# Kernel optimization log

Measured on AMD Instinct MI355X. Metric: run time of the kernel, lower is better.

## Reference

```python
import jax, jax.numpy as jnp
import numpy as np
from jax.scipy.linalg import expm

DELTA = 0.01  # time step from __init__ delta
B_SZ, U_DIM, DU_DIM, H_DIM, Y_DIM = 512, 1024, 512, 2048, 1024


def setup_inputs() -> dict:
    key = jax.random.key(0)
    ks = jax.random.split(key, 6)
    inv_sqrt = lambda fan_in: 1.0 / np.sqrt(fan_in)
    u = jax.random.normal(ks[0], (B_SZ, U_DIM), jnp.float32)
    du = jax.random.normal(ks[1], (B_SZ, DU_DIM), jnp.float32)
    # torch.nn.Linear default init: U(-1/sqrt(fan_in), 1/sqrt(fan_in))
    W = jax.random.uniform(ks[2], (H_DIM, H_DIM), jnp.float32, -inv_sqrt(H_DIM), inv_sqrt(H_DIM))
    Bw = jax.random.uniform(ks[3], (H_DIM, U_DIM + DU_DIM), jnp.float32, -inv_sqrt(U_DIM + DU_DIM), inv_sqrt(U_DIM + DU_DIM))
    Cw = jax.random.uniform(ks[4], (Y_DIM, H_DIM), jnp.float32, -inv_sqrt(H_DIM), inv_sqrt(H_DIM))
    h = jax.random.normal(ks[5], (1, H_DIM), jnp.float32)
    return {"u": u, "du": du, "W": W, "Bw": Bw, "Cw": Cw, "h": h}


def reference(u, du, W, Bw, Cw, h):
    # Antisymmetric part of W
    A = 0.5 * (W - W.T)                                    # (H,H)
    A_expm = expm(A * DELTA)                               # (H,H) matrix exponential
    rec = h @ A_expm.T                                     # (1,H) recurrent term: F.linear(h, A_expm)
    A_inv = jnp.linalg.inv(A)                              # (H,H)
    # B(cat([du, u])) : (B, H)
    b = jnp.concatenate([du, u], axis=1) @ Bw.T
    # M = A^{-1} (expm(A*delta) - I); input term = M @ b^T per sample -> b @ M^T
    M = A_inv @ (A_expm - jnp.eye(H_DIM, dtype=A.dtype))   # (H,H)
    inp = b @ M.T                                          # (B,H)
    h_new = rec + inp                                      # broadcast (1,H)+(B,H) -> (B,H)
    y = h_new @ Cw.T                                       # (B,Y)
    return y
```

## Files before the change

kernel.cpp:

```cpp
#include <hip/hip_runtime.h>
#include <hip/hip_bf16.h>


#define B_SZ 512
#define U_DIM 1024
#define DU_DIM 512
#define H_DIM 2048
#define Y_DIM 1024
#define K_CAT 1536
#define DELTA_F 0.01f

typedef __hip_bfloat16 bf16;
using bf16x8f = __attribute__((ext_vector_type(8))) short;
using f32x4   = __attribute__((ext_vector_type(4))) float;

__device__ __forceinline__ short f2bs(float x) {
  union { bf16 b; short s; } u; u.b = __float2bfloat16(x); return u.s;
}
__device__ __forceinline__ int4 pack8(const float4 v0, const float4 v1) {
  union { short s[8]; int4 i; } o;
  o.s[0] = f2bs(v0.x); o.s[1] = f2bs(v0.y); o.s[2] = f2bs(v0.z); o.s[3] = f2bs(v0.w);
  o.s[4] = f2bs(v1.x); o.s[5] = f2bs(v1.y); o.s[6] = f2bs(v1.z); o.s[7] = f2bs(v1.w);
  return o.i;
}

#define LDP 72
#define LDS_SHORTS (2 * 32 * LDP + 2 * 64 * LDP)

#define NB (H_DIM * K_CAT / 8)

__global__ __launch_bounds__(256) void k1(const float* __restrict__ W, const float* __restrict__ h,
                                          const float* __restrict__ Bw, float* __restrict__ wh,
                                          float* __restrict__ wtp, short* __restrict__ Bwb) {
  const int b = blockIdx.x;
  if (b < 512) {
    const int lane = threadIdx.x & 63, wave = threadIdx.x >> 6;
    const int row = b * 4 + wave;
    const float* wr = W + (size_t)row * H_DIM;
    float s = 0.f;
#pragma unroll
    for (int it = 0; it < 8; it++) {
      int k = it * 256 + lane * 4;
      float4 a = *(const float4*)(wr + k);
      float4 hv = *(const float4*)(h + k);
      s += a.x * hv.x + a.y * hv.y + a.z * hv.z + a.w * hv.w;
    }
#pragma unroll
    for (int off = 32; off > 0; off >>= 1) s += __shfl_down(s, off);
    if (lane == 0) wh[row] = s;
  } else if (b < 768) {
    const int e = b - 512;
    const int colg = e & 7, rowg = e >> 3;
    const int k = colg * 256 + threadIdx.x;
    float s = 0.f;
    const float* base = W + (size_t)rowg * 64 * H_DIM + k;
#pragma unroll 8
    for (int i = 0; i < 64; i++) s += base[(size_t)i * H_DIM] * h[rowg * 64 + i];
    wtp[rowg * H_DIM + k] = s;
  } else {
    for (int g = (b - 768) * 256 + threadIdx.x; g < NB; g += 256 * 256) {
      int e = g * 8;
      *(int4*)(Bwb + e) = pack8(*(const float4*)(Bw + e), *(const float4*)(Bw + e + 4));
    }
  }
}

__device__ __forceinline__ void k2_tile(short* lds, float* recf, const float* __restrict__ du,
                                        const float* __restrict__ u, const short* __restrict__ B,
                                        const float* __restrict__ h, const float* __restrict__ wh,
                                        const float* __restrict__ wtp, short* __restrict__ out,
                                        int mt, int nt) {
  const int KDIM = K_CAT;
  short* As0 = lds;
  short* Bs0 = lds + 2 * 32 * LDP;
  const int tid = threadIdx.x;
  const int lane = tid & 63, wave = tid >> 6;
  const int wm = wave >> 1, wn = wave & 1;
  const int row0 = mt * 32, col0 = nt * 64;
  const int rA = tid >> 3, kc = (tid & 7) * 8;
  f32x4 acc[2] = {};
  int4 pa, pb1, pb2;
  auto ldA = [&](int kt) -> int4 {
    int col = kt * 64 + kc;
    const float* p = (col < DU_DIM) ? du + (size_t)(row0 + rA) * DU_DIM + col
                                    : u + (size_t)(row0 + rA) * U_DIM + (col - DU_DIM);
    return pack8(*(const float4*)p, *(const float4*)(p + 4));
  };
  auto ldB1 = [&](int kt) { return *(const int4*)(B + (size_t)(col0 + rA) * KDIM + kt * 64 + kc); };
  auto ldB2 = [&](int kt) { return *(const int4*)(B + (size_t)(col0 + rA + 32) * KDIM + kt * 64 + kc); };
  pa = ldA(0); pb1 = ldB1(0); pb2 = ldB2(0);
  *(int4*)&As0[rA * LDP + kc] = pa;
  *(int4*)&Bs0[rA * LDP + kc] = pb1;
  *(int4*)&Bs0[(rA + 32) * LDP + kc] = pb2;
  const int NT = KDIM / 64;
  const int kq = (lane >> 4) * 8, rm = lane & 15;
  for (int kt = 0; kt < NT; kt++) {
    const int cur = kt & 1;
    if (kt + 1 < NT) { pa = ldA(kt + 1); pb1 = ldB1(kt + 1); pb2 = ldB2(kt + 1); }
    __syncthreads();
    const short* Ac = As0 + cur * (32 * LDP);
    const short* Bc = Bs0 + cur * (64 * LDP);
    bf16x8f af[2], bfr[2][2];
#pragma unroll
    for (int ks = 0; ks < 2; ks++) {
      af[ks] = *(const bf16x8f*)&Ac[(wm * 16 + rm) * LDP + ks * 32 + kq];
#pragma unroll
      for (int j = 0; j < 2; j++)
        bfr[ks][j] = *(const bf16x8f*)&Bc[(wn * 32 + 16 * j + rm) * LDP + ks * 32 + kq];
    }
#pragma unroll
    for (int ks = 0; ks < 2; ks++)
#pragma unroll
      for (int j = 0; j < 2; j++)
        acc[j] = __builtin_amdgcn_mfma_f32_16x16x32_bf16(af[ks], bfr[ks][j], acc[j], 0, 0, 0);
    if (kt + 1 < NT) {
      short* An = As0 + (cur ^ 1) * (32 * LDP);
      short* Bn = Bs0 + (cur ^ 1) * (64 * LDP);
      *(int4*)&An[rA * LDP + kc] = pa;
      *(int4*)&Bn[rA * LDP + kc] = pb1;
      *(int4*)&Bn[(rA + 32) * LDP + kc] = pb2;
      __syncthreads();
    }
  }
  if (tid < 64) {
    int gc = col0 + tid;
    float s = 0.f;
#pragma unroll
    for (int p = 0; p < 32; p++) s += wtp[p * H_DIM + gc];
    recf[tid] = h[gc] + 0.005f * (wh[gc] - s);
  }
  __syncthreads();
  const int quad = lane >> 4;
#pragma unroll
  for (int j = 0; j < 2; j++) {
    int gc = col0 + wn * 32 + 16 * j + rm;
#pragma unroll
    for (int r = 0; r < 4; r++) {
      int gr = row0 + wm * 16 + quad * 4 + r;
      out[(size_t)gr * H_DIM + gc] = f2bs(recf[gc - col0] + DELTA_F * acc[j][r]);
    }
  }
}

__global__ __launch_bounds__(256) void k2(const float* __restrict__ du, const float* __restrict__ u,
                                          const short* __restrict__ Bwb, const float* __restrict__ h,
                                          const float* __restrict__ wh, const float* __restrict__ wtp,
                                          short* __restrict__ bb, const float* __restrict__ Cw,
                                          short* __restrict__ Cwb) {
  __shared__ __align__(16) short lds[LDS_SHORTS];
  __shared__ float recf[64];
  const int b = blockIdx.x;
  if (b < 512) {
    k2_tile(lds, recf, du, u, Bwb, h, wh, wtp, bb, b >> 5, b & 31);
  } else {
    int g = (b - 512) * 256 + threadIdx.x;
    int e = g * 8;
    *(int4*)(Cwb + e) = pack8(*(const float4*)(Cw + e), *(const float4*)(Cw + e + 4));
    e = (g + 131072) * 8;
    *(int4*)(Cwb + e) = pack8(*(const float4*)(Cw + e), *(const float4*)(Cw + e + 4));
  }
}

__global__ __launch_bounds__(256) void k3(const short* __restrict__ A, const short* __restrict__ B,
                                          float* __restrict__ y) {
  __shared__ __align__(16) short lds[LDS_SHORTS];
  const int KDIM = H_DIM;
  short* As0 = lds;
  short* Bs0 = lds + 2 * 32 * LDP;
  const int tid = threadIdx.x;
  const int lane = tid & 63, wave = tid >> 6;
  const int wm = wave >> 1, wn = wave & 1;
  const int mt = blockIdx.x >> 5, nt = blockIdx.x & 31;
  const int row0 = mt * 32, col0 = nt * 32;
  const int rA = tid >> 3, kc = (tid & 7) * 8;
  f32x4 acc = {};
  int4 pa, pb;
  auto ldA = [&](int kt) { return *(const int4*)(A + (size_t)(row0 + rA) * KDIM + kt * 64 + kc); };
  auto ldB = [&](int kt) { return *(const int4*)(B + (size_t)(col0 + rA) * KDIM + kt * 64 + kc); };
  pa = ldA(0); pb = ldB(0);
  *(int4*)&As0[rA * LDP + kc] = pa;
  *(int4*)&Bs0[rA * LDP + kc] = pb;
  const int NT = KDIM / 64;
  const int kq = (lane >> 4) * 8, rm = lane & 15;
  for (int kt = 0; kt < NT; kt++) {
    const int cur = kt & 1;
    if (kt + 1 < NT) { pa = ldA(kt + 1); pb = ldB(kt + 1); }
    __syncthreads();
    const short* Ac = As0 + cur * (32 * LDP);
    const short* Bc = Bs0 + cur * (32 * LDP);
#pragma unroll
    for (int ks = 0; ks < 2; ks++) {
      bf16x8f af = *(const bf16x8f*)&Ac[(wm * 16 + rm) * LDP + ks * 32 + kq];
      bf16x8f bf = *(const bf16x8f*)&Bc[(wn * 16 + rm) * LDP + ks * 32 + kq];
      acc = __builtin_amdgcn_mfma_f32_16x16x32_bf16(af, bf, acc, 0, 0, 0);
    }
    if (kt + 1 < NT) {
      short* An = As0 + (cur ^ 1) * (32 * LDP);
      short* Bn = Bs0 + (cur ^ 1) * (32 * LDP);
      *(int4*)&An[rA * LDP + kc] = pa;
      *(int4*)&Bn[rA * LDP + kc] = pb;
      __syncthreads();
    }
  }
  const int quad = lane >> 4;
  int gc = col0 + wn * 16 + rm;
#pragma unroll
  for (int r = 0; r < 4; r++) {
    int gr = row0 + wm * 16 + quad * 4 + r;
    y[(size_t)gr * Y_DIM + gc] = acc[r];
  }
}

extern "C" void kernel_launch(void* const* d_in, const int* in_sizes, int n_in,
                              void* d_out, int out_size, void* d_ws, size_t ws_size,
                              hipStream_t stream) {
  const float* u  = (const float*)d_in[0];
  const float* du = (const float*)d_in[1];
  const float* W  = (const float*)d_in[2];
  const float* Bw = (const float*)d_in[3];
  const float* Cw = (const float*)d_in[4];
  const float* h  = (const float*)d_in[5];
  float* y = (float*)d_out;

  char* w = (char*)d_ws;
  size_t off = 0;
  short* Bwb = (short*)(w + off); off += (size_t)H_DIM * K_CAT * sizeof(short);
  short* Cwb = (short*)(w + off); off += (size_t)Y_DIM * H_DIM * sizeof(short);
  short* bb  = (short*)(w + off); off += (size_t)B_SZ * H_DIM * sizeof(short);
  float* wh  = (float*)(w + off); off += H_DIM * sizeof(float);
  float* wtp = (float*)(w + off); off += 32 * H_DIM * sizeof(float);
  if (ws_size < off) return;

  k1<<<1024, 256, 0, stream>>>(W, h, Bw, wh, wtp, Bwb);
  k2<<<1024, 256, 0, stream>>>(du, u, Bwb, h, wh, wtp, bb, Cw, Cwb);
  k3<<<512, 256, 0, stream>>>(bb, Cwb, y);
}
```

Measured before the change: 122.8 us.

## Replace LDS-tiled GEMMs with per-wave register-prefetch MFMA tiles and precast inputs

Both GEMMs drop the shared-memory double-buffered block tiling. Each wave now computes its own 32x32 output tile, loading bf16 fragments straight from global memory into registers with a one-step prefetch and no barriers. The concatenated du/u input is cast to bf16 once in k1, and the Cw conversion is folded into fewer blocks. In exchange this removes LDS traffic and syncs but loses sharing of operands across waves, raising global/L2 traffic, and launches fewer blocks.

```diff
diff --git a/kernel.cpp b/kernel.cpp
--- a/kernel.cpp
+++ b/kernel.cpp
@@ -24,14 +24,15 @@
   return o.i;
 }
 
-#define LDP 72
-#define LDS_SHORTS (2 * 32 * LDP + 2 * 64 * LDP)
-
-#define NB (H_DIM * K_CAT / 8)
+#define NB   (H_DIM * K_CAT / 8)
+#define NCAT (B_SZ * K_CAT / 8)
+#define NC   (Y_DIM * H_DIM / 8)
 
 __global__ __launch_bounds__(256) void k1(const float* __restrict__ W, const float* __restrict__ h,
-                                          const float* __restrict__ Bw, float* __restrict__ wh,
-                                          float* __restrict__ wtp, short* __restrict__ Bwb) {
+                                          const float* __restrict__ Bw, const float* __restrict__ du,
+                                          const float* __restrict__ u, float* __restrict__ wh,
+                                          float* __restrict__ wtp, short* __restrict__ Bwb,
+                                          short* __restrict__ catb) {
   const int b = blockIdx.x;
   if (b < 512) {
     const int lane = threadIdx.x & 63, wave = threadIdx.x >> 6;
@@ -58,157 +59,116 @@
     for (int i = 0; i < 64; i++) s += base[(size_t)i * H_DIM] * h[rowg * 64 + i];
     wtp[rowg * H_DIM + k] = s;
   } else {
-    for (int g = (b - 768) * 256 + threadIdx.x; g < NB; g += 256 * 256) {
-      int e = g * 8;
-      *(int4*)(Bwb + e) = pack8(*(const float4*)(Bw + e), *(const float4*)(Bw + e + 4));
+    for (int g = (b - 768) * 256 + threadIdx.x; g < NB + NCAT; g += 256 * 256) {
+      if (g < NB) {
+        int e = g * 8;
+        *(int4*)(Bwb + e) = pack8(*(const float4*)(Bw + e), *(const float4*)(Bw + e + 4));
+      } else {
+        int g2 = g - NB;
+        int row = g2 / 192, c = g2 - row * 192;
+        const float* src = (c < 64) ? du + (size_t)row * DU_DIM + c * 8
+                                    : u + (size_t)row * U_DIM + (c - 64) * 8;
+        *(int4*)(catb + (size_t)row * K_CAT + c * 8) =
+            pack8(*(const float4*)src, *(const float4*)(src + 4));
+      }
     }
   }
 }
 
-__device__ __forceinline__ void k2_tile(short* lds, float* recf, const float* __restrict__ du,
-                                        const float* __restrict__ u, const short* __restrict__ B,
-                                        const float* __restrict__ h, const float* __restrict__ wh,
-                                        const float* __restrict__ wtp, short* __restrict__ out,
-                                        int mt, int nt) {
-  const int KDIM = K_CAT;
-  short* As0 = lds;
-  short* Bs0 = lds + 2 * 32 * LDP;
-  const int tid = threadIdx.x;
-  const int lane = tid & 63, wave = tid >> 6;
-  const int wm = wave >> 1, wn = wave & 1;
-  const int row0 = mt * 32, col0 = nt * 64;
-  const int rA = tid >> 3, kc = (tid & 7) * 8;
-  f32x4 acc[2] = {};
-  int4 pa, pb1, pb2;
-  auto ldA = [&](int kt) -> int4 {
-    int col = kt * 64 + kc;
-    const float* p = (col < DU_DIM) ? du + (size_t)(row0 + rA) * DU_DIM + col
-                                    : u + (size_t)(row0 + rA) * U_DIM + (col - DU_DIM);
-    return pack8(*(const float4*)p, *(const float4*)(p + 4));
-  };
-  auto ldB1 = [&](int kt) { return *(const int4*)(B + (size_t)(col0 + rA) * KDIM + kt * 64 + kc); };
-  auto ldB2 = [&](int kt) { return *(const int4*)(B + (size_t)(col0 + rA + 32) * KDIM + kt * 64 + kc); };
-  pa = ldA(0); pb1 = ldB1(0); pb2 = ldB2(0);
-  *(int4*)&As0[rA * LDP + kc] = pa;
-  *(int4*)&Bs0[rA * LDP + kc] = pb1;
-  *(int4*)&Bs0[(rA + 32) * LDP + kc] = pb2;
-  const int NT = KDIM / 64;
-  const int kq = (lane >> 4) * 8, rm = lane & 15;
-  for (int kt = 0; kt < NT; kt++) {
-    const int cur = kt & 1;
-    if (kt + 1 < NT) { pa = ldA(kt + 1); pb1 = ldB1(kt + 1); pb2 = ldB2(kt + 1); }
-    __syncthreads();
-    const short* Ac = As0 + cur * (32 * LDP);
-    const short* Bc = Bs0 + cur * (64 * LDP);
-    bf16x8f af[2], bfr[2][2];
+#define MFMA __builtin_amdgcn_mfma_f32_16x16x32_bf16
+template <int KDIM>
+__device__ __forceinline__ void gemm_wave(const short* __restrict__ A, const short* __restrict__ B,
+                                          int row0, int col0, int rm, int kq, f32x4* acc) {
+  const short* pa0 = A + (size_t)(row0 + rm) * KDIM + kq;
+  const short* pa1 = pa0 + (size_t)16 * KDIM;
+  const short* pb0 = B + (size_t)(col0 + rm) * KDIM + kq;
+  const short* pb1 = pb0 + (size_t)16 * KDIM;
+  constexpr int NS = KDIM / 32;
+  bf16x8f a0 = *(const bf16x8f*)(pa0),      a1 = *(const bf16x8f*)(pa1);
+  bf16x8f b0 = *(const bf16x8f*)(pb0),      b1 = *(const bf16x8f*)(pb1);
+  bf16x8f a2 = *(const bf16x8f*)(pa0 + 32), a3 = *(const bf16x8f*)(pa1 + 32);
+  bf16x8f b2 = *(const bf16x8f*)(pb0 + 32), b3 = *(const bf16x8f*)(pb1 + 32);
+#pragma unroll 2
+  for (int kt = 2; kt < NS; kt += 2) {
+    const int o = kt * 32;
+    bf16x8f na0 = *(const bf16x8f*)(pa0 + o),      na1 = *(const bf16x8f*)(pa1 + o);
+    bf16x8f nb0 = *(const bf16x8f*)(pb0 + o),      nb1 = *(const bf16x8f*)(pb1 + o);
+    bf16x8f na2 = *(const bf16x8f*)(pa0 + o + 32), na3 = *(const bf16x8f*)(pa1 + o + 32);
+    bf16x8f nb2 = *(const bf16x8f*)(pb0 + o + 32), nb3 = *(const bf16x8f*)(pb1 + o + 32);
+    acc[0] = MFMA(a0, b0, acc[0], 0, 0, 0); acc[1] = MFMA(a0, b1, acc[1], 0, 0, 0);
+    acc[2] = MFMA(a1, b0, acc[2], 0, 0, 0); acc[3] = MFMA(a1, b1, acc[3], 0, 0, 0);
+    acc[0] = MFMA(a2, b2, acc[0], 0, 0, 0); acc[1] = MFMA(a2, b3, acc[1], 0, 0, 0);
+    acc[2] = MFMA(a3, b2, acc[2], 0, 0, 0); acc[3] = MFMA(a3, b3, acc[3], 0, 0, 0);
+    a0 = na0; a1 = na1; b0 = nb0; b1 = nb1;
+    a2 = na2; a3 = na3; b2 = nb2; b3 = nb3;
+  }
+  acc[0] = MFMA(a0, b0, acc[0], 0, 0, 0); acc[1] = MFMA(a0, b1, acc[1], 0, 0, 0);
+  acc[2] = MFMA(a1, b0, acc[2], 0, 0, 0); acc[3] = MFMA(a1, b1, acc[3], 0, 0, 0);
+  acc[0] = MFMA(a2, b2, acc[0], 0, 0, 0); acc[1] = MFMA(a2, b3, acc[1], 0, 0, 0);
+  acc[2] = MFMA(a3, b2, acc[2], 0, 0, 0); acc[3] = MFMA(a3, b3, acc[3], 0, 0, 0);
+}
+
+__global__ __launch_bounds__(256) void k2(const short* __restrict__ catb, const short* __restrict__ Bwb,
+                                          const float* __restrict__ h, const float* __restrict__ wh,
+                                          const float* __restrict__ wtp, short* __restrict__ bb,
+                                          const float* __restrict__ Cw, short* __restrict__ Cwb) {
+  const int b = blockIdx.x;
+  if (b < 256) {
+    const int lane = threadIdx.x & 63, wave = threadIdx.x >> 6;
+    const int t = b * 4 + wave;
+    const int mt = t >> 6, nt = t & 63;
+    const int row0 = mt * 32, col0 = nt * 32;
+    const int rm = lane & 15, quad = lane >> 4, kq = quad * 8;
+    f32x4 acc[4] = {};
+    gemm_wave<K_CAT>(catb, Bwb, row0, col0, rm, kq, acc);
+    float recv[2];
 #pragma unroll
-    for (int ks = 0; ks < 2; ks++) {
-      af[ks] = *(const bf16x8f*)&Ac[(wm * 16 + rm) * LDP + ks * 32 + kq];
+    for (int j = 0; j < 2; j++) {
+      int c = col0 + 16 * j + rm;
+      float s = 0.f;
+#pragma unroll
+      for (int p = 0; p < 32; p++) s += wtp[p * H_DIM + c];
+      recv[j] = h[c] + 0.005f * (wh[c] - s);
+    }
+#pragma unroll
+    for (int i = 0; i < 2; i++)
 #pragma unroll
       for (int j = 0; j < 2; j++)
-        bfr[ks][j] = *(const bf16x8f*)&Bc[(wn * 32 + 16 * j + rm) * LDP + ks * 32 + kq];
+#pragma unroll
+        for (int r = 0; r < 4; r++) {
+          int gr = row0 + 16 * i + quad * 4 + r;
+          int gc = col0 + 16 * j + rm;
+          bb[(size_t)gr * H_DIM + gc] = f2bs(recv[j] + DELTA_F * acc[i * 2 + j][r]);
+        }
+  } else {
+    int g0 = (b - 256) * 256 + threadIdx.x;
+#pragma unroll
+    for (int it = 0; it < 8; it++) {
+      int e = (g0 + it * 32768) * 8;
+      *(int4*)(Cwb + e) = pack8(*(const float4*)(Cw + e), *(const float4*)(Cw + e + 4));
     }
-#pragma unroll
-    for (int ks = 0; ks < 2; ks++)
-#pragma unroll
-      for (int j = 0; j < 2; j++)
-        acc[j] = __builtin_amdgcn_mfma_f32_16x16x32_bf16(af[ks], bfr[ks][j], acc[j], 0, 0, 0);
-    if (kt + 1 < NT) {
-      short* An = As0 + (cur ^ 1) * (32 * LDP);
-      short* Bn = Bs0 + (cur ^ 1) * (64 * LDP);
-      *(int4*)&An[rA * LDP + kc] = pa;
-      *(int4*)&Bn[rA * LDP + kc] = pb1;
-      *(int4*)&Bn[(rA + 32) * LDP + kc] = pb2;
-      __syncthreads();
-    }
-  }
-  if (tid < 64) {
-    int gc = col0 + tid;
-    float s = 0.f;
-#pragma unroll
-    for (int p = 0; p < 32; p++) s += wtp[p * H_DIM + gc];
-    recf[tid] = h[gc] + 0.005f * (wh[gc] - s);
-  }
-  __syncthreads();
-  const int quad = lane >> 4;
-#pragma unroll
-  for (int j = 0; j < 2; j++) {
-    int gc = col0 + wn * 32 + 16 * j + rm;
-#pragma unroll
-    for (int r = 0; r < 4; r++) {
-      int gr = row0 + wm * 16 + quad * 4 + r;
-      out[(size_t)gr * H_DIM + gc] = f2bs(recf[gc - col0] + DELTA_F * acc[j][r]);
-    }
-  }
-}
-
-__global__ __launch_bounds__(256) void k2(const float* __restrict__ du, const float* __restrict__ u,
-                                          const short* __restrict__ Bwb, const float* __restrict__ h,
-                                          const float* __restrict__ wh, const float* __restrict__ wtp,
-                                          short* __restrict__ bb, const float* __restrict__ Cw,
-                                          short* __restrict__ Cwb) {
-  __shared__ __align__(16) short lds[LDS_SHORTS];
-  __shared__ float recf[64];
-  const int b = blockIdx.x;
-  if (b < 512) {
-    k2_tile(lds, recf, du, u, Bwb, h, wh, wtp, bb, b >> 5, b & 31);
-  } else {
-    int g = (b - 512) * 256 + threadIdx.x;
-    int e = g * 8;
-    *(int4*)(Cwb + e) = pack8(*(const float4*)(Cw + e), *(const float4*)(Cw + e + 4));
-    e = (g + 131072) * 8;
-    *(int4*)(Cwb + e) = pack8(*(const float4*)(Cw + e), *(const float4*)(Cw + e + 4));
   }
 }
 
 __global__ __launch_bounds__(256) void k3(const short* __restrict__ A, const short* __restrict__ B,
                                           float* __restrict__ y) {
-  __shared__ __align__(16) short lds[LDS_SHORTS];
-  const int KDIM = H_DIM;
-  short* As0 = lds;
-  short* Bs0 = lds + 2 * 32 * LDP;
-  const int tid = threadIdx.x;
-  const int lane = tid & 63, wave = tid >> 6;
-  const int wm = wave >> 1, wn = wave & 1;
-  const int mt = blockIdx.x >> 5, nt = blockIdx.x & 31;
+  const int lane = threadIdx.x & 63, wave = threadIdx.x >> 6;
+  const int t = blockIdx.x * 4 + wave;
+  const int mt = t >> 5, nt = t & 31;
   const int row0 = mt * 32, col0 = nt * 32;
-  const int rA = tid >> 3, kc = (tid & 7) * 8;
-  f32x4 acc = {};
-  int4 pa, pb;
-  auto ldA = [&](int kt) { return *(const int4*)(A + (size_t)(row0 + rA) * KDIM + kt * 64 + kc); };
-  auto ldB = [&](int kt) { return *(const int4*)(B + (size_t)(col0 + rA) * KDIM + kt * 64 + kc); };
-  pa = ldA(0); pb = ldB(0);
-  *(int4*)&As0[rA * LDP + kc] = pa;
-  *(int4*)&Bs0[rA * LDP + kc] = pb;
-  const int NT = KDIM / 64;
-  const int kq = (lane >> 4) * 8, rm = lane & 15;
-  for (int kt = 0; kt < NT; kt++) {
-    const int cur = kt & 1;
-    if (kt + 1 < NT) { pa = ldA(kt + 1); pb = ldB(kt + 1); }
-    __syncthreads();
-    const short* Ac = As0 + cur * (32 * LDP);
-    const short* Bc = Bs0 + cur * (32 * LDP);
+  const int rm = lane & 15, quad = lane >> 4, kq = quad * 8;
+  f32x4 acc[4] = {};
+  gemm_wave<H_DIM>(A, B, row0, col0, rm, kq, acc);
 #pragma unroll
-    for (int ks = 0; ks < 2; ks++) {
-      bf16x8f af = *(const bf16x8f*)&Ac[(wm * 16 + rm) * LDP + ks * 32 + kq];
-      bf16x8f bf = *(const bf16x8f*)&Bc[(wn * 16 + rm) * LDP + ks * 32 + kq];
-      acc = __builtin_amdgcn_mfma_f32_16x16x32_bf16(af, bf, acc, 0, 0, 0);
-    }
-    if (kt + 1 < NT) {
-      short* An = As0 + (cur ^ 1) * (32 * LDP);
-      short* Bn = Bs0 + (cur ^ 1) * (32 * LDP);
-      *(int4*)&An[rA * LDP + kc] = pa;
-      *(int4*)&Bn[rA * LDP + kc] = pb;
-      __syncthreads();
-    }
-  }
-  const int quad = lane >> 4;
-  int gc = col0 + wn * 16 + rm;
+  for (int i = 0; i < 2; i++)
 #pragma unroll
-  for (int r = 0; r < 4; r++) {
-    int gr = row0 + wm * 16 + quad * 4 + r;
-    y[(size_t)gr * Y_DIM + gc] = acc[r];
-  }
+    for (int j = 0; j < 2; j++)
+#pragma unroll
+      for (int r = 0; r < 4; r++) {
+        int gr = row0 + 16 * i + quad * 4 + r;
+        int gc = col0 + 16 * j + rm;
+        y[(size_t)gr * Y_DIM + gc] = acc[i * 2 + j][r];
+      }
 }
 
 extern "C" void kernel_launch(void* const* d_in, const int* in_sizes, int n_in,
@@ -224,14 +184,15 @@
 
   char* w = (char*)d_ws;
   size_t off = 0;
-  short* Bwb = (short*)(w + off); off += (size_t)H_DIM * K_CAT * sizeof(short);
-  short* Cwb = (short*)(w + off); off += (size_t)Y_DIM * H_DIM * sizeof(short);
-  short* bb  = (short*)(w + off); off += (size_t)B_SZ * H_DIM * sizeof(short);
-  float* wh  = (float*)(w + off); off += H_DIM * sizeof(float);
-  float* wtp = (float*)(w + off); off += 32 * H_DIM * sizeof(float);
+  short* Bwb  = (short*)(w + off); off += (size_t)H_DIM * K_CAT * sizeof(short);
+  short* Cwb  = (short*)(w + off); off += (size_t)Y_DIM * H_DIM * sizeof(short);
+  short* bb   = (short*)(w + off); off += (size_t)B_SZ * H_DIM * sizeof(short);
+  short* catb = (short*)(w + off); off += (size_t)B_SZ * K_CAT * sizeof(short);
+  float* wh   = (float*)(w + off); off += H_DIM * sizeof(float);
+  float* wtp  = (float*)(w + off); off += 32 * H_DIM * sizeof(float);
   if (ws_size < off) return;
 
-  k1<<<1024, 256, 0, stream>>>(W, h, Bw, wh, wtp, Bwb);
-  k2<<<1024, 256, 0, stream>>>(du, u, Bwb, h, wh, wtp, bb, Cw, Cwb);
-  k3<<<512, 256, 0, stream>>>(bb, Cwb, y);
+  k1<<<1024, 256, 0, stream>>>(W, h, Bw, du, u, wh, wtp, Bwb, catb);
+  k2<<<384, 256, 0, stream>>>(catb, Bwb, h, wh, wtp, bb, Cw, Cwb);
+  k3<<<128, 256, 0, stream>>>(bb, Cwb, y);
 }
```

Result: slower. 143.9 us (+17.3%).
